# Kernel tuning notes

Hardware: AMD Instinct MI355X
Metric: run time of the kernel (lower is better)

Reference implementation:

```python
import jax, jax.numpy as jnp
import numpy as np

N_NODES = 20000
N_EDGES = 640000
NUM_COUNTS = 64
NUM_FEATS = 128


def setup_inputs() -> dict:
    key = jax.random.key(0)
    k1, k2, k3, k4, k5 = jax.random.split(key, 5)
    cnt = jax.random.uniform(k1, (N_EDGES, NUM_COUNTS), dtype=jnp.float32)
    embedding = jax.random.normal(k2, (N_NODES, NUM_FEATS), dtype=jnp.float32)
    importance = jax.random.normal(k3, (NUM_COUNTS, NUM_FEATS), dtype=jnp.float32)
    src = jax.random.randint(k4, (N_EDGES,), 0, N_NODES, dtype=jnp.int32)
    # ensure every node has >=1 incoming edge so the normalization divide is well-defined
    dst = jax.random.permutation(k5, jnp.arange(N_EDGES, dtype=jnp.int32) % N_NODES)
    return {"cnt": cnt, "embedding": embedding, "importance": importance, "src": src, "dst": dst}


def reference(cnt, embedding, importance, src, dst):
    # weight = softmax over the num_counts axis (dim=0)
    weight = jax.nn.softmax(importance, axis=0)            # [C, F]
    edge_score = cnt @ weight                               # [E, F] dense GEMM
    msgs = embedding[src] * edge_score                      # [E, F] u_mul_e
    new_embedding = jax.ops.segment_sum(msgs, dst, num_segments=N_NODES)      # [N, F]
    node_score = jax.ops.segment_sum(edge_score, dst, num_segments=N_NODES)   # [N, F]
    return new_embedding / node_score
```

## Files before the change

kernel.cpp:

```cpp
#include <hip/hip_runtime.h>
#include <hip/hip_bf16.h>
#include <stdint.h>

#define NN 20000
#define NE 640000
#define NC 64
#define NF 128
#define CAP 32
#define ESTRIDE 132
#define NPW 5
#define WPB 4

typedef __attribute__((ext_vector_type(8))) short short8;
typedef __attribute__((ext_vector_type(8))) __bf16 bf16x8;
typedef __attribute__((ext_vector_type(2))) __bf16 bf16x2;
typedef __attribute__((ext_vector_type(4))) float floatx4;
typedef __attribute__((ext_vector_type(4))) unsigned int uintx4;

static __device__ __forceinline__ unsigned short f2bf(float f) {
  union { float f; unsigned int i; } v; v.f = f;
  unsigned int x = v.i;
  x += 0x7fffu + ((x >> 16) & 1u);
  return (unsigned short)(x >> 16);
}

static __device__ __forceinline__ unsigned int pk2(float a, float b) {
#if __has_builtin(__builtin_amdgcn_cvt_pk_bf16_f32)
  bf16x2 r = __builtin_amdgcn_cvt_pk_bf16_f32(a, b);
  return __builtin_bit_cast(unsigned int, r);
#else
  return (unsigned int)f2bf(a) | ((unsigned int)f2bf(b) << 16);
#endif
}

static __device__ __forceinline__ short8 cvt8(floatx4 lo, floatx4 hi) {
  uintx4 u;
  u.x = pk2(lo[0], lo[1]); u.y = pk2(lo[2], lo[3]);
  u.z = pk2(hi[0], hi[1]); u.w = pk2(hi[2], hi[3]);
  return __builtin_bit_cast(short8, u);
}

static __device__ __forceinline__ float frcp(float x) {
#if __has_builtin(__builtin_amdgcn_rcpf)
  return __builtin_amdgcn_rcpf(x);
#else
  return 1.0f / x;
#endif
}

__global__ void softpack_kernel(const float* __restrict__ imp,
                                unsigned short* __restrict__ wpack) {
  __shared__ float w_s[NC][NF];
  int f = threadIdx.x;
  float v[NC];
  float mx = -1e30f;
#pragma unroll
  for (int c = 0; c < NC; ++c) { v[c] = imp[c * NF + f]; mx = fmaxf(mx, v[c]); }
  float s = 0.f;
#pragma unroll
  for (int c = 0; c < NC; ++c) { v[c] = __expf(v[c] - mx); s += v[c]; }
  float inv = 1.0f / s;
#pragma unroll
  for (int c = 0; c < NC; ++c) w_s[c][f] = v[c] * inv;
  __syncthreads();
#pragma unroll
  for (int idx = 0; idx < 8192; idx += 128) {
    int i2 = idx + f;
    int j  = i2 & 7;
    int l  = (i2 >> 3) & 63;
    int ks = (i2 >> 9) & 1;
    int nt = i2 >> 10;
    int k = ks * 32 + (l >> 4) * 8 + j;
    int n = nt * 16 + (l & 15);
    wpack[i2] = f2bf(w_s[k][n]);
  }
}

__global__ void bin_kernel(const int* __restrict__ dst,
                           int* __restrict__ counts,
                           int* __restrict__ elist,
                           int cstride) {
  int e = blockIdx.x * 256 + threadIdx.x;
  if (e < NE) {
    int n = dst[e];
    int slot = atomicAdd(&counts[(size_t)n * cstride], 1);
    if (slot < CAP) elist[n * CAP + slot] = e;
  }
}

__global__ __launch_bounds__(256) void node_kernel(
    const float* __restrict__ cnt,
    const float* __restrict__ emb,
    const int* __restrict__ srcp,
    const int* __restrict__ elist,
    const unsigned short* __restrict__ wpack,
    float* __restrict__ out)
{
  __shared__ float es_s[WPB][16 * ESTRIDE];
  __shared__ int eids_s[WPB][2][CAP];
  __shared__ int srcs_s[WPB][2][CAP];

  const int tid = threadIdx.x;
  const int wid = tid >> 6;
  const int lane = tid & 63;
  const int m = lane & 15;
  const int q = lane >> 4;
  const int base = (blockIdx.x * WPB + wid) * NPW;
  float* es = es_s[wid];

  short8 wf[8][2];
#pragma unroll
  for (int nt = 0; nt < 8; ++nt)
#pragma unroll
    for (int ks = 0; ks < 2; ++ks)
      wf[nt][ks] = *(const short8*)(wpack + ((nt * 2 + ks) * 64 + lane) * 8);

  if (lane < CAP) {
    int e0 = elist[(size_t)base * CAP + lane];
    eids_s[wid][0][lane] = e0;
    srcs_s[wid][0][lane] = srcp[e0];
  }

  for (int i = 0; i < NPW; ++i) {
    const int buf = i & 1;
    const int node = base + i;
    const bool do_pre = (i + 1 < NPW) && (lane < CAP);

    int pe = 0, ps = 0;
    if (do_pre) pe = elist[(size_t)(node + 1) * CAP + lane];

    asm volatile("s_waitcnt lgkmcnt(0)" ::: "memory");

    int eid0 = eids_s[wid][buf][m];
    int eid1 = eids_s[wid][buf][16 + m];

    float ea[8], sa[8];
#pragma unroll
    for (int j = 0; j < 8; ++j) { ea[j] = 0.f; sa[j] = 0.f; }

#pragma unroll
    for (int h = 0; h < 2; ++h) {
      const float* crow = cnt + (size_t)(h ? eid1 : eid0) * NC + q * 8;
      floatx4 c0 = *(const floatx4*)(crow);
      floatx4 c1 = *(const floatx4*)(crow + 4);
      floatx4 c2 = *(const floatx4*)(crow + 32);
      floatx4 c3 = *(const floatx4*)(crow + 36);
      short8 a0 = cvt8(c0, c1);
      short8 a1 = cvt8(c2, c3);

      floatx4 acc[8];
#pragma unroll
      for (int nt = 0; nt < 8; ++nt)
#pragma unroll
        for (int r = 0; r < 4; ++r) acc[nt][r] = 0.f;
#pragma unroll
      for (int nt = 0; nt < 8; ++nt) {
        acc[nt] = __builtin_amdgcn_mfma_f32_16x16x32_bf16(
            __builtin_bit_cast(bf16x8, a0), __builtin_bit_cast(bf16x8, wf[nt][0]),
            acc[nt], 0, 0, 0);
        acc[nt] = __builtin_amdgcn_mfma_f32_16x16x32_bf16(
            __builtin_bit_cast(bf16x8, a1), __builtin_bit_cast(bf16x8, wf[nt][1]),
            acc[nt], 0, 0, 0);
      }

#pragma unroll
      for (int nt = 0; nt < 8; ++nt)
#pragma unroll
        for (int r = 0; r < 4; ++r)
          es[(q * 4 + r) * ESTRIDE + nt * 16 + m] = acc[nt][r];

      if (h == 0 && do_pre) ps = srcp[pe];

      asm volatile("s_waitcnt lgkmcnt(0)" ::: "memory");

#pragma unroll
      for (int t = 0; t < 4; ++t) {
        int el = q + 4 * t;
        floatx4 p0 = *(const floatx4*)&es[el * ESTRIDE + m * 8];
        floatx4 p1 = *(const floatx4*)&es[el * ESTRIDE + m * 8 + 4];
        int s = srcs_s[wid][buf][h * 16 + el];
        const float* erow = emb + (size_t)s * NF + m * 8;
        floatx4 e0 = *(const floatx4*)erow;
        floatx4 e1 = *(const floatx4*)(erow + 4);
#pragma unroll
        for (int j = 0; j < 4; ++j) {
          ea[j]     = fmaf(p0[j], e0[j], ea[j]);
          ea[j + 4] = fmaf(p1[j], e1[j], ea[j + 4]);
          sa[j]     += p0[j];
          sa[j + 4] += p1[j];
        }
      }
      asm volatile("" ::: "memory");
    }

    if (do_pre) { eids_s[wid][buf ^ 1][lane] = pe; srcs_s[wid][buf ^ 1][lane] = ps; }

#pragma unroll
    for (int j = 0; j < 8; ++j) {
      ea[j] += __shfl_xor(ea[j], 16, 64);
      ea[j] += __shfl_xor(ea[j], 32, 64);
      sa[j] += __shfl_xor(sa[j], 16, 64);
      sa[j] += __shfl_xor(sa[j], 32, 64);
    }

    if (lane < 16) {
      floatx4 o0, o1;
#pragma unroll
      for (int p = 0; p < 4; ++p) {
        o0[p] = ea[p] * frcp(sa[p]);
        o1[p] = ea[p + 4] * frcp(sa[p + 4]);
      }
      float* op = out + (size_t)node * NF + lane * 8;
      *(floatx4*)op = o0;
      *(floatx4*)(op + 4) = o1;
    }
  }
}

extern "C" void kernel_launch(void* const* d_in, const int* in_sizes, int n_in,
                              void* d_out, int out_size, void* d_ws, size_t ws_size,
                              hipStream_t stream) {
  const float* cnt = (const float*)d_in[0];
  const float* emb = (const float*)d_in[1];
  const float* imp = (const float*)d_in[2];
  const int* src = (const int*)d_in[3];
  const int* dst = (const int*)d_in[4];
  float* out = (float*)d_out;

  char* ws = (char*)d_ws;
  unsigned short* wpack = (unsigned short*)(ws);

  const size_t need_padded = 16384 + (size_t)NN * 32 + (size_t)NN * CAP * 4;
  int cstride;
  int* counts;
  int* elist;
  if (ws_size >= need_padded) {
    cstride = 8;
    counts = (int*)(ws + 16384);
    elist  = (int*)(ws + 16384 + (size_t)NN * 32);
  } else {
    cstride = 1;
    counts = (int*)(ws + 16384);
    elist  = (int*)(ws + 98304);
  }

  hipMemsetAsync(counts, 0, (size_t)NN * cstride * sizeof(int), stream);
  softpack_kernel<<<1, NF, 0, stream>>>(imp, wpack);
  bin_kernel<<<(NE + 255) / 256, 256, 0, stream>>>(dst, counts, elist, cstride);
  node_kernel<<<NN / (WPB * NPW), 256, 0, stream>>>(cnt, emb, src, elist, wpack, out);
}
```

Before: 301.0 us.

## Stream cnt rows via async global-to-LDS loads and consume MFMA output in registers

Edge rows of cnt are now fetched with global_load_lds into a double-buffered, XOR-swizzled LDS tile, so the next half-node's rows load while the current half's MFMAs run. The LDS round trip that transposed the edge-score tile is gone: MFMA accumulators are multiplied directly against embedding elements gathered per row, and edge ids and src ids move through shuffles instead of shared memory. This removes LDS stores and loads and the extra waits, at the cost of scalar 4-byte embedding gathers in place of 16-byte vector loads, and the output is now written with scalar stores from all lanes.

```diff
diff --git a/kernel.cpp b/kernel.cpp
--- a/kernel.cpp
+++ b/kernel.cpp
@@ -7,9 +7,9 @@
 #define NC 64
 #define NF 128
 #define CAP 32
-#define ESTRIDE 132
 #define NPW 5
 #define WPB 4
+#define NSTEP (2 * NPW)
 
 typedef __attribute__((ext_vector_type(8))) short short8;
 typedef __attribute__((ext_vector_type(8))) __bf16 bf16x8;
@@ -47,6 +47,11 @@
   return 1.0f / x;
 #endif
 }
+
+#define GLOAD_LDS(gp, lp)                                                      \
+  __builtin_amdgcn_global_load_lds(                                           \
+      (const __attribute__((address_space(1))) void*)(gp),                     \
+      (__attribute__((address_space(3))) void*)(lp), 16, 0, 0)
 
 __global__ void softpack_kernel(const float* __restrict__ imp,
                                 unsigned short* __restrict__ wpack) {
@@ -96,9 +101,7 @@
     const unsigned short* __restrict__ wpack,
     float* __restrict__ out)
 {
-  __shared__ float es_s[WPB][16 * ESTRIDE];
-  __shared__ int eids_s[WPB][2][CAP];
-  __shared__ int srcs_s[WPB][2][CAP];
+  __shared__ float cnt_s[WPB][2][16 * NC];
 
   const int tid = threadIdx.x;
   const int wid = tid >> 6;
@@ -106,7 +109,6 @@
   const int m = lane & 15;
   const int q = lane >> 4;
   const int base = (blockIdx.x * WPB + wid) * NPW;
-  float* es = es_s[wid];
 
   short8 wf[8][2];
 #pragma unroll
@@ -115,104 +117,102 @@
     for (int ks = 0; ks < 2; ++ks)
       wf[nt][ks] = *(const short8*)(wpack + ((nt * 2 + ks) * 64 + lane) * 8);
 
-  if (lane < CAP) {
-    int e0 = elist[(size_t)base * CAP + lane];
-    eids_s[wid][0][lane] = e0;
-    srcs_s[wid][0][lane] = srcp[e0];
-  }
-
-  for (int i = 0; i < NPW; ++i) {
-    const int buf = i & 1;
-    const int node = base + i;
-    const bool do_pre = (i + 1 < NPW) && (lane < CAP);
-
-    int pe = 0, ps = 0;
-    if (do_pre) pe = elist[(size_t)(node + 1) * CAP + lane];
-
-    asm volatile("s_waitcnt lgkmcnt(0)" ::: "memory");
-
-    int eid0 = eids_s[wid][buf][m];
-    int eid1 = eids_s[wid][buf][16 + m];
-
-    float ea[8], sa[8];
-#pragma unroll
-    for (int j = 0; j < 8; ++j) { ea[j] = 0.f; sa[j] = 0.f; }
-
-#pragma unroll
-    for (int h = 0; h < 2; ++h) {
-      const float* crow = cnt + (size_t)(h ? eid1 : eid0) * NC + q * 8;
-      floatx4 c0 = *(const floatx4*)(crow);
-      floatx4 c1 = *(const floatx4*)(crow + 4);
-      floatx4 c2 = *(const floatx4*)(crow + 32);
-      floatx4 c3 = *(const floatx4*)(crow + 36);
-      short8 a0 = cvt8(c0, c1);
-      short8 a1 = cvt8(c2, c3);
-
-      floatx4 acc[8];
+  int e_cur = elist[(size_t)base * CAP + (lane & 31)];
+  int s_cur = srcp[e_cur];
+  int pe = 0, ps = 0;
+
+#pragma unroll
+  for (int j = 0; j < 4; ++j) {
+    int rl = 4 * j + q;
+    int eid = __shfl(e_cur, rl);
+    int cs = m ^ (rl & 7);
+    GLOAD_LDS(cnt + (size_t)eid * NC + cs * 4, &cnt_s[wid][0][j * 256]);
+  }
+
+  float ea[8], sa[8];
+
+#pragma unroll
+  for (int s = 0; s < NSTEP; ++s) {
+    const int h = s & 1;
+    const int node = base + (s >> 1);
+    const int cbuf = s & 1;
+    const bool more = (s + 1 < NSTEP);
+
+    if (h == 0) {
+#pragma unroll
+      for (int t = 0; t < 8; ++t) { ea[t] = 0.f; sa[t] = 0.f; }
+      if (s + 2 < NSTEP) pe = elist[(size_t)(node + 1) * CAP + (lane & 31)];
+    } else if (more) {
+      ps = srcp[pe];
+    }
+
+    if (more) {
+#pragma unroll
+      for (int j = 0; j < 4; ++j) {
+        int rl = 4 * j + q;
+        int eid = __shfl(h ? pe : e_cur, (h ? 0 : 16) + rl);
+        int cs = m ^ (rl & 7);
+        GLOAD_LDS(cnt + (size_t)eid * NC + cs * 4,
+                  &cnt_s[wid][cbuf ^ 1][j * 256]);
+      }
+      asm volatile("s_waitcnt vmcnt(4)" ::: "memory");
+    } else {
+      asm volatile("s_waitcnt vmcnt(0)" ::: "memory");
+    }
+
+    const float* cb = cnt_s[wid][cbuf];
+    const int sw = m & 7;
+    const int rb = m * NC;
+    floatx4 c0 = *(const floatx4*)&cb[rb + ((2 * q)     ^ sw) * 4];
+    floatx4 c1 = *(const floatx4*)&cb[rb + ((2 * q + 1) ^ sw) * 4];
+    floatx4 c2 = *(const floatx4*)&cb[rb + ((8 + 2 * q) ^ sw) * 4];
+    floatx4 c3 = *(const floatx4*)&cb[rb + ((9 + 2 * q) ^ sw) * 4];
+    short8 a0 = cvt8(c0, c1);
+    short8 a1 = cvt8(c2, c3);
+
+    floatx4 acc[8];
+#pragma unroll
+    for (int nt = 0; nt < 8; ++nt) {
+#pragma unroll
+      for (int r = 0; r < 4; ++r) acc[nt][r] = 0.f;
+      acc[nt] = __builtin_amdgcn_mfma_f32_16x16x32_bf16(
+          __builtin_bit_cast(bf16x8, a0), __builtin_bit_cast(bf16x8, wf[nt][0]),
+          acc[nt], 0, 0, 0);
+      acc[nt] = __builtin_amdgcn_mfma_f32_16x16x32_bf16(
+          __builtin_bit_cast(bf16x8, a1), __builtin_bit_cast(bf16x8, wf[nt][1]),
+          acc[nt], 0, 0, 0);
+    }
+
+#pragma unroll
+    for (int nt = 0; nt < 8; ++nt)
+#pragma unroll
+      for (int r = 0; r < 4; ++r) sa[nt] += acc[nt][r];
+
+#pragma unroll
+    for (int r = 0; r < 4; ++r) {
+      int sv = __shfl(s_cur, h * 16 + 4 * q + r);
+      const float* er = emb + (size_t)sv * NF + m;
 #pragma unroll
       for (int nt = 0; nt < 8; ++nt)
-#pragma unroll
-        for (int r = 0; r < 4; ++r) acc[nt][r] = 0.f;
-#pragma unroll
-      for (int nt = 0; nt < 8; ++nt) {
-        acc[nt] = __builtin_amdgcn_mfma_f32_16x16x32_bf16(
-            __builtin_bit_cast(bf16x8, a0), __builtin_bit_cast(bf16x8, wf[nt][0]),
-            acc[nt], 0, 0, 0);
-        acc[nt] = __builtin_amdgcn_mfma_f32_16x16x32_bf16(
-            __builtin_bit_cast(bf16x8, a1), __builtin_bit_cast(bf16x8, wf[nt][1]),
-            acc[nt], 0, 0, 0);
+        ea[nt] = fmaf(acc[nt][r], er[nt * 16], ea[nt]);
+    }
+
+    if (h == 1) {
+#pragma unroll
+      for (int t = 0; t < 8; ++t) {
+        ea[t] += __shfl_xor(ea[t], 16, 64);
+        ea[t] += __shfl_xor(ea[t], 32, 64);
+        sa[t] += __shfl_xor(sa[t], 16, 64);
+        sa[t] += __shfl_xor(sa[t], 32, 64);
       }
-
-#pragma unroll
-      for (int nt = 0; nt < 8; ++nt)
-#pragma unroll
-        for (int r = 0; r < 4; ++r)
-          es[(q * 4 + r) * ESTRIDE + nt * 16 + m] = acc[nt][r];
-
-      if (h == 0 && do_pre) ps = srcp[pe];
-
-      asm volatile("s_waitcnt lgkmcnt(0)" ::: "memory");
-
-#pragma unroll
-      for (int t = 0; t < 4; ++t) {
-        int el = q + 4 * t;
-        floatx4 p0 = *(const floatx4*)&es[el * ESTRIDE + m * 8];
-        floatx4 p1 = *(const floatx4*)&es[el * ESTRIDE + m * 8 + 4];
-        int s = srcs_s[wid][buf][h * 16 + el];
-        const float* erow = emb + (size_t)s * NF + m * 8;
-        floatx4 e0 = *(const floatx4*)erow;
-        floatx4 e1 = *(const floatx4*)(erow + 4);
-#pragma unroll
-        for (int j = 0; j < 4; ++j) {
-          ea[j]     = fmaf(p0[j], e0[j], ea[j]);
-          ea[j + 4] = fmaf(p1[j], e1[j], ea[j + 4]);
-          sa[j]     += p0[j];
-          sa[j + 4] += p1[j];
-        }
-      }
-      asm volatile("" ::: "memory");
-    }
-
-    if (do_pre) { eids_s[wid][buf ^ 1][lane] = pe; srcs_s[wid][buf ^ 1][lane] = ps; }
-
-#pragma unroll
-    for (int j = 0; j < 8; ++j) {
-      ea[j] += __shfl_xor(ea[j], 16, 64);
-      ea[j] += __shfl_xor(ea[j], 32, 64);
-      sa[j] += __shfl_xor(sa[j], 16, 64);
-      sa[j] += __shfl_xor(sa[j], 32, 64);
-    }
-
-    if (lane < 16) {
-      floatx4 o0, o1;
-#pragma unroll
-      for (int p = 0; p < 4; ++p) {
-        o0[p] = ea[p] * frcp(sa[p]);
-        o1[p] = ea[p + 4] * frcp(sa[p + 4]);
-      }
-      float* op = out + (size_t)node * NF + lane * 8;
-      *(floatx4*)op = o0;
-      *(floatx4*)(op + 4) = o1;
+      float e0 = (q & 2) ? ((q & 1) ? ea[6] : ea[4]) : ((q & 1) ? ea[2] : ea[0]);
+      float e1 = (q & 2) ? ((q & 1) ? ea[7] : ea[5]) : ((q & 1) ? ea[3] : ea[1]);
+      float d0 = (q & 2) ? ((q & 1) ? sa[6] : sa[4]) : ((q & 1) ? sa[2] : sa[0]);
+      float d1 = (q & 2) ? ((q & 1) ? sa[7] : sa[5]) : ((q & 1) ? sa[3] : sa[1]);
+      float* op = out + (size_t)node * NF;
+      op[(2 * q) * 16 + m]     = e0 * frcp(d0);
+      op[(2 * q + 1) * 16 + m] = e1 * frcp(d1);
+      if (more) { e_cur = pe; s_cur = ps; }
     }
   }
 }
```

Result: no change. 300.5 us (-0.2%).
